# Optimization experiments

Measured on AMD Instinct MI355X. Metric: run time of the kernel, lower is better.

## Reference

```python
import jax, jax.numpy as jnp
import numpy as np

MIN_NORM = 1e-15

def mobius_add(x, y, c):
    # geoopt mobius_add with curvature k = -c (Poincare ball)
    x2 = jnp.sum(x * x, axis=-1, keepdims=True)
    y2 = jnp.sum(y * y, axis=-1, keepdims=True)
    xy = jnp.sum(x * y, axis=-1, keepdims=True)
    num = (1.0 + 2.0 * c * xy + c * y2) * x + (1.0 - c * x2) * y
    den = 1.0 + 2.0 * c * xy + c * c * x2 * y2
    return num / jnp.maximum(den, MIN_NORM)


def setup_inputs() -> dict:
    key = jax.random.key(0)
    k1, k2, k3 = jax.random.split(key, 3)
    B, D, K = 4096, 128, 256
    # points in the Poincare ball (norm << 1)
    x = jax.random.normal(k1, (B, D), jnp.float32) * 0.01
    # p_k = expmap0(randn*1e-5) ~= randn*1e-5 for tiny norms
    p_k = jax.random.normal(k2, (K, D), jnp.float32) * 1e-5
    stdv = (6.0 / (K + D)) ** 0.5
    a_k = jax.random.uniform(k3, (K, D), jnp.float32, -stdv, stdv)
    return {"x": x, "p_k": p_k, "a_k": a_k}


def reference(x, p_k, a_k):
    c = 1.0
    sqrt_c = c ** 0.5
    xq = x[:, None, :]                       # (B, 1, D)
    mpx = mobius_add(-p_k, xq, c)            # (B, K, D)
    mpx_sqnorm = jnp.maximum(jnp.sum(mpx * mpx, axis=-1), MIN_NORM)  # (B, K)
    mpx_dot_a = jnp.sum(mpx * a_k, axis=-1)                          # (B, K)
    a_norm = jnp.maximum(jnp.linalg.norm(a_k, axis=-1), MIN_NORM)    # (K,)
    num = 2.0 * sqrt_c * mpx_dot_a
    den = jnp.maximum((1.0 - c * mpx_sqnorm) * a_norm, MIN_NORM)
    distance = jnp.arcsinh(num / den) / sqrt_c
    return 2.0 * a_norm * distance           # (B, K) logits
```

## Files before the change

### kernel.cpp

```cpp
#include <hip/hip_runtime.h>
#include <hip/hip_bf16.h>
#include <math.h>

#define B_SZ 4096
#define D_SZ 128
#define K_SZ 256
#define MT   64
#define NT   64
#define LSTR 136
#define MIN_NORM 1e-15f

typedef __attribute__((ext_vector_type(8))) short  short8;
typedef __attribute__((ext_vector_type(4))) float  floatx4;

static __device__ __forceinline__ unsigned short f2bf(float f) {
    union { float f; unsigned int u; } v; v.f = f;
    unsigned int u = v.u;
    u += 0x7FFFu + ((u >> 16) & 1u);
    return (unsigned short)(u >> 16);
}
static __device__ __forceinline__ float bf2f(unsigned short h) {
    union { unsigned int u; float f; } v; v.u = ((unsigned int)h) << 16;
    return v.f;
}

__global__ __launch_bounds__(256) void mobius_mlr_kernel(
        const float* __restrict__ x, const float* __restrict__ p,
        const float* __restrict__ a, float* __restrict__ out) {
    __shared__ __align__(16) unsigned short lx[MT * LSTR];
    __shared__ __align__(16) unsigned short lp[NT * LSTR];
    __shared__ __align__(16) unsigned short la[NT * LSTR];
    __shared__ float xsq[MT];
    __shared__ float p2s[NT], pas[NT], ans[NT];

    const int tid = threadIdx.x;
    const int mb0 = blockIdx.x * MT;
    const int nb0 = blockIdx.y * NT;

    const float4* xg = (const float4*)x + (size_t)mb0 * (D_SZ / 4);
    const float4* pg = (const float4*)p + (size_t)nb0 * (D_SZ / 4);
    const float4* ag = (const float4*)a + (size_t)nb0 * (D_SZ / 4);
    #pragma unroll
    for (int j = 0; j < 8; ++j) {
        int idx = tid + j * 256;
        int row = idx >> 5;
        int c4  = idx & 31;
        float4 vx = xg[row * 32 + c4];
        float4 vp = pg[row * 32 + c4];
        float4 va = ag[row * 32 + c4];
        ushort4 sx = make_ushort4(f2bf(vx.x), f2bf(vx.y), f2bf(vx.z), f2bf(vx.w));
        ushort4 sp = make_ushort4(f2bf(vp.x), f2bf(vp.y), f2bf(vp.z), f2bf(vp.w));
        ushort4 sa = make_ushort4(f2bf(va.x), f2bf(va.y), f2bf(va.z), f2bf(va.w));
        *(ushort4*)&lx[row * LSTR + c4 * 4] = sx;
        *(ushort4*)&lp[row * LSTR + c4 * 4] = sp;
        *(ushort4*)&la[row * LSTR + c4 * 4] = sa;
    }
    __syncthreads();

    if (tid < 64) {
        float s = 0.f;
        const short8* r = (const short8*)&lx[tid * LSTR];
        #pragma unroll
        for (int i = 0; i < 16; ++i) {
            short8 v = r[i];
            #pragma unroll
            for (int e = 0; e < 8; ++e) { float f = bf2f((unsigned short)v[e]); s += f * f; }
        }
        xsq[tid] = s;
    } else if (tid < 128) {
        int k = tid - 64;
        float sp = 0.f, spa = 0.f;
        const short8* rp = (const short8*)&lp[k * LSTR];
        const short8* ra = (const short8*)&la[k * LSTR];
        #pragma unroll
        for (int i = 0; i < 16; ++i) {
            short8 vp = rp[i], va = ra[i];
            #pragma unroll
            for (int e = 0; e < 8; ++e) {
                float fp = bf2f((unsigned short)vp[e]);
                float fa = bf2f((unsigned short)va[e]);
                sp += fp * fp; spa += fp * fa;
            }
        }
        p2s[k] = sp; pas[k] = spa;
    } else if (tid < 192) {
        int k = tid - 128;
        float sa = 0.f;
        const short8* ra = (const short8*)&la[k * LSTR];
        #pragma unroll
        for (int i = 0; i < 16; ++i) {
            short8 va = ra[i];
            #pragma unroll
            for (int e = 0; e < 8; ++e) { float f = bf2f((unsigned short)va[e]); sa += f * f; }
        }
        ans[k] = fmaxf(sqrtf(sa), MIN_NORM);
    }

    const int lane = tid & 63;
    const int wv   = tid >> 6;
    const int quad = lane >> 4;
    const int r16  = lane & 15;
    const int arow = wv * 16 + r16;

    floatx4 accp[4], acca[4];
    #pragma unroll
    for (int j = 0; j < 4; ++j) {
        accp[j] = (floatx4){0.f, 0.f, 0.f, 0.f};
        acca[j] = (floatx4){0.f, 0.f, 0.f, 0.f};
    }

    #pragma unroll
    for (int dc = 0; dc < 4; ++dc) {
        int d0 = dc * 32 + quad * 8;
        short8 af = *(const short8*)&lx[arow * LSTR + d0];
        #pragma unroll
        for (int j = 0; j < 4; ++j) {
            short8 bp = *(const short8*)&lp[(j * 16 + r16) * LSTR + d0];
            short8 ba = *(const short8*)&la[(j * 16 + r16) * LSTR + d0];
            accp[j] = __builtin_amdgcn_mfma_f32_16x16x32_bf16(af, bp, accp[j], 0, 0, 0);
            acca[j] = __builtin_amdgcn_mfma_f32_16x16x32_bf16(af, ba, acca[j], 0, 0, 0);
        }
    }
    __syncthreads();

    #pragma unroll
    for (int j = 0; j < 4; ++j) {
        int coll = j * 16 + r16;
        float p2v = p2s[coll];
        float pav = pas[coll];
        float anv = ans[coll];
        #pragma unroll
        for (int r = 0; r < 4; ++r) {
            int rowl = wv * 16 + quad * 4 + r;
            float x2v = xsq[rowl];
            float pdx = accp[j][r];
            float xda = acca[j][r];
            float alpha = 1.0f - 2.0f * pdx + x2v;
            float beta  = 1.0f - p2v;
            float den   = fmaxf(1.0f - 2.0f * pdx + p2v * x2v, MIN_NORM);
            float invd  = 1.0f / den;
            float sqn   = (alpha * alpha * p2v - 2.0f * alpha * beta * pdx
                           + beta * beta * x2v) * invd * invd;
            sqn = fmaxf(sqn, MIN_NORM);
            float mda = (beta * xda - alpha * pav) * invd;
            float dden = fmaxf((1.0f - sqn) * anv, MIN_NORM);
            float dist = asinhf(2.0f * mda / dden);
            out[(size_t)(mb0 + rowl) * K_SZ + (nb0 + coll)] = 2.0f * anv * dist;
        }
    }
}

extern "C" void kernel_launch(void* const* d_in, const int* in_sizes, int n_in,
                              void* d_out, int out_size, void* d_ws, size_t ws_size,
                              hipStream_t stream) {
    const float* x = (const float*)d_in[0];
    const float* p = (const float*)d_in[1];
    const float* a = (const float*)d_in[2];
    float* out = (float*)d_out;
    dim3 grid(B_SZ / MT, K_SZ / NT);
    mobius_mlr_kernel<<<grid, dim3(256), 0, stream>>>(x, p, a, out);
}
```

Before: 67.27 us.

## Shrink tiles to 32x32, split row reductions across lanes, use fast math

Tile size drops from 64x64 to 32x32, so the grid has four times as many blocks, and each wave now computes one 16x16 MFMA tile pair instead of four. The prologue norm reductions are split across four lanes per row and combined with shuffles, and the a-norm is fused into the p-reduction pass. The epilogue replaces divisions with hardware reciprocals and asinhf with a log/sqrt formula. The goal is more parallelism and a shorter serial prologue. In exchange, each block re-loads x, p and a more often, asinh loses accuracy for negative arguments, and the global loads are less amortized.

```diff
diff --git a/kernel.cpp b/kernel.cpp
--- a/kernel.cpp
+++ b/kernel.cpp
@@ -5,8 +5,8 @@
 #define B_SZ 4096
 #define D_SZ 128
 #define K_SZ 256
-#define MT   64
-#define NT   64
+#define MT   32
+#define NT   32
 #define LSTR 136
 #define MIN_NORM 1e-15f
 
@@ -41,112 +41,102 @@
     const float4* pg = (const float4*)p + (size_t)nb0 * (D_SZ / 4);
     const float4* ag = (const float4*)a + (size_t)nb0 * (D_SZ / 4);
     #pragma unroll
-    for (int j = 0; j < 8; ++j) {
+    for (int j = 0; j < 4; ++j) {
         int idx = tid + j * 256;
         int row = idx >> 5;
         int c4  = idx & 31;
-        float4 vx = xg[row * 32 + c4];
-        float4 vp = pg[row * 32 + c4];
-        float4 va = ag[row * 32 + c4];
-        ushort4 sx = make_ushort4(f2bf(vx.x), f2bf(vx.y), f2bf(vx.z), f2bf(vx.w));
-        ushort4 sp = make_ushort4(f2bf(vp.x), f2bf(vp.y), f2bf(vp.z), f2bf(vp.w));
-        ushort4 sa = make_ushort4(f2bf(va.x), f2bf(va.y), f2bf(va.z), f2bf(va.w));
-        *(ushort4*)&lx[row * LSTR + c4 * 4] = sx;
-        *(ushort4*)&lp[row * LSTR + c4 * 4] = sp;
-        *(ushort4*)&la[row * LSTR + c4 * 4] = sa;
+        float4 vx = xg[idx];
+        float4 vp = pg[idx];
+        float4 va = ag[idx];
+        *(ushort4*)&lx[row * LSTR + c4 * 4] =
+            make_ushort4(f2bf(vx.x), f2bf(vx.y), f2bf(vx.z), f2bf(vx.w));
+        *(ushort4*)&lp[row * LSTR + c4 * 4] =
+            make_ushort4(f2bf(vp.x), f2bf(vp.y), f2bf(vp.z), f2bf(vp.w));
+        *(ushort4*)&la[row * LSTR + c4 * 4] =
+            make_ushort4(f2bf(va.x), f2bf(va.y), f2bf(va.z), f2bf(va.w));
     }
     __syncthreads();
 
-    if (tid < 64) {
+    if (tid < 128) {
+        int row = tid >> 2, q = tid & 3;
+        const short8* r = (const short8*)&lx[row * LSTR + q * 32];
         float s = 0.f;
-        const short8* r = (const short8*)&lx[tid * LSTR];
         #pragma unroll
-        for (int i = 0; i < 16; ++i) {
+        for (int i = 0; i < 4; ++i) {
             short8 v = r[i];
             #pragma unroll
             for (int e = 0; e < 8; ++e) { float f = bf2f((unsigned short)v[e]); s += f * f; }
         }
-        xsq[tid] = s;
-    } else if (tid < 128) {
-        int k = tid - 64;
-        float sp = 0.f, spa = 0.f;
-        const short8* rp = (const short8*)&lp[k * LSTR];
-        const short8* ra = (const short8*)&la[k * LSTR];
+        s += __shfl_xor(s, 1);
+        s += __shfl_xor(s, 2);
+        if (q == 0) xsq[row] = s;
+    } else {
+        int t = tid - 128;
+        int row = t >> 2, q = t & 3;
+        const short8* rp = (const short8*)&lp[row * LSTR + q * 32];
+        const short8* ra = (const short8*)&la[row * LSTR + q * 32];
+        float sp = 0.f, spa = 0.f, sa2 = 0.f;
         #pragma unroll
-        for (int i = 0; i < 16; ++i) {
+        for (int i = 0; i < 4; ++i) {
             short8 vp = rp[i], va = ra[i];
             #pragma unroll
             for (int e = 0; e < 8; ++e) {
                 float fp = bf2f((unsigned short)vp[e]);
                 float fa = bf2f((unsigned short)va[e]);
-                sp += fp * fp; spa += fp * fa;
+                sp += fp * fp; spa += fp * fa; sa2 += fa * fa;
             }
         }
-        p2s[k] = sp; pas[k] = spa;
-    } else if (tid < 192) {
-        int k = tid - 128;
-        float sa = 0.f;
-        const short8* ra = (const short8*)&la[k * LSTR];
-        #pragma unroll
-        for (int i = 0; i < 16; ++i) {
-            short8 va = ra[i];
-            #pragma unroll
-            for (int e = 0; e < 8; ++e) { float f = bf2f((unsigned short)va[e]); sa += f * f; }
+        sp  += __shfl_xor(sp, 1);  sp  += __shfl_xor(sp, 2);
+        spa += __shfl_xor(spa, 1); spa += __shfl_xor(spa, 2);
+        sa2 += __shfl_xor(sa2, 1); sa2 += __shfl_xor(sa2, 2);
+        if (q == 0) {
+            p2s[row] = sp; pas[row] = spa;
+            ans[row] = fmaxf(sqrtf(sa2), MIN_NORM);
         }
-        ans[k] = fmaxf(sqrtf(sa), MIN_NORM);
     }
 
     const int lane = tid & 63;
     const int wv   = tid >> 6;
+    const int mi   = wv & 1;
+    const int ni   = wv >> 1;
     const int quad = lane >> 4;
     const int r16  = lane & 15;
-    const int arow = wv * 16 + r16;
 
-    floatx4 accp[4], acca[4];
-    #pragma unroll
-    for (int j = 0; j < 4; ++j) {
-        accp[j] = (floatx4){0.f, 0.f, 0.f, 0.f};
-        acca[j] = (floatx4){0.f, 0.f, 0.f, 0.f};
-    }
-
+    floatx4 accp = {0.f, 0.f, 0.f, 0.f};
+    floatx4 acca = {0.f, 0.f, 0.f, 0.f};
     #pragma unroll
     for (int dc = 0; dc < 4; ++dc) {
         int d0 = dc * 32 + quad * 8;
-        short8 af = *(const short8*)&lx[arow * LSTR + d0];
-        #pragma unroll
-        for (int j = 0; j < 4; ++j) {
-            short8 bp = *(const short8*)&lp[(j * 16 + r16) * LSTR + d0];
-            short8 ba = *(const short8*)&la[(j * 16 + r16) * LSTR + d0];
-            accp[j] = __builtin_amdgcn_mfma_f32_16x16x32_bf16(af, bp, accp[j], 0, 0, 0);
-            acca[j] = __builtin_amdgcn_mfma_f32_16x16x32_bf16(af, ba, acca[j], 0, 0, 0);
-        }
+        short8 af = *(const short8*)&lx[(mi * 16 + r16) * LSTR + d0];
+        short8 bp = *(const short8*)&lp[(ni * 16 + r16) * LSTR + d0];
+        short8 ba = *(const short8*)&la[(ni * 16 + r16) * LSTR + d0];
+        accp = __builtin_amdgcn_mfma_f32_16x16x32_bf16(af, bp, accp, 0, 0, 0);
+        acca = __builtin_amdgcn_mfma_f32_16x16x32_bf16(af, ba, acca, 0, 0, 0);
     }
     __syncthreads();
 
+    const int coll = ni * 16 + r16;
+    const float p2v = p2s[coll];
+    const float pav = pas[coll];
+    const float anv = ans[coll];
     #pragma unroll
-    for (int j = 0; j < 4; ++j) {
-        int coll = j * 16 + r16;
-        float p2v = p2s[coll];
-        float pav = pas[coll];
-        float anv = ans[coll];
-        #pragma unroll
-        for (int r = 0; r < 4; ++r) {
-            int rowl = wv * 16 + quad * 4 + r;
-            float x2v = xsq[rowl];
-            float pdx = accp[j][r];
-            float xda = acca[j][r];
-            float alpha = 1.0f - 2.0f * pdx + x2v;
-            float beta  = 1.0f - p2v;
-            float den   = fmaxf(1.0f - 2.0f * pdx + p2v * x2v, MIN_NORM);
-            float invd  = 1.0f / den;
-            float sqn   = (alpha * alpha * p2v - 2.0f * alpha * beta * pdx
-                           + beta * beta * x2v) * invd * invd;
-            sqn = fmaxf(sqn, MIN_NORM);
-            float mda = (beta * xda - alpha * pav) * invd;
-            float dden = fmaxf((1.0f - sqn) * anv, MIN_NORM);
-            float dist = asinhf(2.0f * mda / dden);
-            out[(size_t)(mb0 + rowl) * K_SZ + (nb0 + coll)] = 2.0f * anv * dist;
-        }
+    for (int r = 0; r < 4; ++r) {
+        int rowl = mi * 16 + quad * 4 + r;
+        float x2v = xsq[rowl];
+        float pdx = accp[r];
+        float xda = acca[r];
+        float alpha = 1.0f - 2.0f * pdx + x2v;
+        float beta  = 1.0f - p2v;
+        float den   = fmaxf(1.0f - 2.0f * pdx + p2v * x2v, MIN_NORM);
+        float invd  = __builtin_amdgcn_rcpf(den);
+        float sqn   = (alpha * alpha * p2v - 2.0f * alpha * beta * pdx
+                       + beta * beta * x2v) * invd * invd;
+        sqn = fmaxf(sqn, MIN_NORM);
+        float mda  = (beta * xda - alpha * pav) * invd;
+        float dden = fmaxf((1.0f - sqn) * anv, MIN_NORM);
+        float z    = 2.0f * mda * __builtin_amdgcn_rcpf(dden);
+        float dist = __logf(z + sqrtf(z * z + 1.0f));
+        out[(size_t)(mb0 + rowl) * K_SZ + (nb0 + coll)] = 2.0f * anv * dist;
     }
 }
 
```

Measured after the change: 63.36 us. 5.8% less time.
